# Performance work log

Hardware: AMD Instinct MI355X
Metric: run time of the kernel (lower is better)

The kernel has to match this reference:

```python
import jax, jax.numpy as jnp
import numpy as np

BETA = 0.05  # module hardcodes self.beta = 0.05 regardless of init arg
K = 4096
D = 512


def setup_inputs() -> dict:
    key = jax.random.key(0)
    k1, k2 = jax.random.split(key)
    latents = jax.random.normal(k1, (32, 1024, D), dtype=jnp.float32)
    # nn.Embedding weight init: normal_(mean=0.8, std=0.1)
    emb_weight = 0.8 + 0.1 * jax.random.normal(k2, (K, D), dtype=jnp.float32)
    return {"latents": latents, "emb_weight": emb_weight}


def reference(latents, emb_weight):
    B, S, Dm = latents.shape
    flat = latents.reshape(-1, Dm)  # [N, D]
    dist = (jnp.sum(flat * flat, axis=1, keepdims=True)
            + jnp.sum(emb_weight * emb_weight, axis=1)
            - 2.0 * jnp.matmul(flat, emb_weight.T))  # [N, K]
    inds = jnp.argmin(dist, axis=1)  # [N]
    quantized = emb_weight[inds].reshape(B, S, Dm)  # gather instead of one-hot matmul

    commitment_loss = jnp.mean((jax.lax.stop_gradient(quantized) - latents) ** 2)
    embedding_loss = jnp.mean((quantized - jax.lax.stop_gradient(latents)) ** 2)
    vq_loss = commitment_loss * BETA + embedding_loss

    # straight-through estimator
    quantized_st = latents + jax.lax.stop_gradient(quantized - latents)

    N = flat.shape[0]
    avg_probs = jnp.zeros((K,), dtype=latents.dtype).at[inds].add(1.0) / N
    perplexity = jnp.exp(-jnp.sum(avg_probs * jnp.log(avg_probs + 1e-10)))

    output_inds = inds.reshape(B, S)
    return (quantized_st, vq_loss, output_inds, emb_weight, perplexity)
```

## Files before the change

### kernel.cpp

```cpp
#include <hip/hip_runtime.h>
#include <cfloat>
#include <cmath>
#include <climits>
#include <cstdint>

#define N_ROWS   32768
#define D_DIM    512
#define K_CODES  4096

#define EPS_GAP  0.008f
#define CAND_WIN 0.02f
#define FLAG_CAP 12000

typedef short s16x8 __attribute__((ext_vector_type(8)));
typedef float f32x4 __attribute__((ext_vector_type(4)));


__device__ __forceinline__ short f2bf_rne(float x) {
    unsigned u = __float_as_uint(x);
    unsigned r = (u + 0x7fffu + ((u >> 16) & 1u)) >> 16;
    return (short)r;
}
__device__ __forceinline__ float bf2f(short b) {
    return __uint_as_float(((unsigned)(unsigned short)b) << 16);
}

__device__ __forceinline__ void gld16(const short* g, short* l) {
    __builtin_amdgcn_global_load_lds(
        reinterpret_cast<const __attribute__((address_space(1))) unsigned int*>(
            reinterpret_cast<uintptr_t>(g)),
        reinterpret_cast<__attribute__((address_space(3))) unsigned int*>(
            (unsigned int)(reinterpret_cast<uintptr_t>(l))),
        16, 0, 0);
}

__device__ __forceinline__ float np_block128_sq(const float* p) {
    float P[16];
    #pragma unroll
    for (int l = 0; l < 16; ++l) {
        float s0 = __fmul_rn(p[0 * 16 + l], p[0 * 16 + l]);
        float s1 = __fmul_rn(p[1 * 16 + l], p[1 * 16 + l]);
        float s2 = __fmul_rn(p[2 * 16 + l], p[2 * 16 + l]);
        float s3 = __fmul_rn(p[3 * 16 + l], p[3 * 16 + l]);
        float s4 = __fmul_rn(p[4 * 16 + l], p[4 * 16 + l]);
        float s5 = __fmul_rn(p[5 * 16 + l], p[5 * 16 + l]);
        float s6 = __fmul_rn(p[6 * 16 + l], p[6 * 16 + l]);
        float s7 = __fmul_rn(p[7 * 16 + l], p[7 * 16 + l]);
        float a01 = __fadd_rn(s0, s1);
        float a23 = __fadd_rn(s2, s3);
        float a45 = __fadd_rn(s4, s5);
        float a67 = __fadd_rn(s6, s7);
        P[l] = __fadd_rn(__fadd_rn(a01, a23), __fadd_rn(a45, a67));
    }
    float T3[8];
    #pragma unroll
    for (int k = 0; k < 8; ++k) T3[k] = __fadd_rn(P[k], P[k + 8]);
    float T6[4];
    #pragma unroll
    for (int k = 0; k < 4; ++k) T6[k] = __fadd_rn(T3[k], T3[k + 4]);
    return __fadd_rn(__fadd_rn(__fadd_rn(T6[0], T6[1]), T6[2]), T6[3]);
}
__device__ __forceinline__ float np_sum512_sq(const float* p) {
    float B0 = np_block128_sq(p);
    float B1 = np_block128_sq(p + 128);
    float B2 = np_block128_sq(p + 256);
    float B3 = np_block128_sq(p + 384);
    return __fadd_rn(__fadd_rn(B0, B1), __fadd_rn(B2, B3));
}

__global__ void vq_convert(const float* __restrict__ lat, const float* __restrict__ emb,
                           short* __restrict__ lat_hi, short* __restrict__ lat_lo,
                           short* __restrict__ emb_hi, short* __restrict__ emb_lo) {
    int i = blockIdx.x * 256 + threadIdx.x;
    const float* src; short *dh, *dl; size_t base;
    if (i < 2097152) { src = lat; dh = lat_hi; dl = lat_lo; base = (size_t)i * 8; }
    else             { src = emb; dh = emb_hi; dl = emb_lo; base = (size_t)(i - 2097152) * 8; }
    float4 a = *(const float4*)(src + base);
    float4 b = *(const float4*)(src + base + 4);
    float x[8] = {a.x, a.y, a.z, a.w, b.x, b.y, b.z, b.w};
    s16x8 hv, lv;
    #pragma unroll
    for (int j = 0; j < 8; ++j) {
        short h = f2bf_rne(x[j]);
        hv[j] = h;
        lv[j] = f2bf_rne(x[j] - bf2f(h));
    }
    *(s16x8*)(dh + base) = hv;
    *(s16x8*)(dl + base) = lv;
}

__global__ void vq_enorm(const float* __restrict__ emb, float* __restrict__ e_norm) {
    int item = blockIdx.x * 4 + (threadIdx.x >> 6);
    int lane = threadIdx.x & 63;
    const float4* s4 = (const float4*)(emb + (size_t)item * D_DIM);
    float4 a = s4[lane];
    float4 b = s4[64 + lane];
    float s = a.x * a.x + a.y * a.y + a.z * a.z + a.w * a.w
            + b.x * b.x + b.y * b.y + b.z * b.z + b.w * b.w;
    #pragma unroll
    for (int off = 32; off > 0; off >>= 1) s += __shfl_down(s, off);
    if (lane == 0) e_norm[item] = s;
}

__device__ __forceinline__ int kswz(int r) { return (r & 3) ^ ((r >> 2) & 3); }

#define BUFS 24576

__global__ __launch_bounds__(1024, 4)
void vq_argmin_mfma(const short* __restrict__ Ah_g, const short* __restrict__ Al_g,
                    const short* __restrict__ Bh_g, const short* __restrict__ Bl_g,
                    const float* __restrict__ e_norm,
                    unsigned short* __restrict__ fidx,
                    int* __restrict__ flagcnt, int* __restrict__ flaglist)
{
    __shared__ short smem[2 * BUFS];

    const int tid = threadIdx.x;
    const int l   = tid & 63;
    const int wid = tid >> 6;
    const int wr  = wid >> 2;
    const int wc  = wid & 3;
    const int l15 = l & 15;
    const int lhi = l >> 4;
    const int row0 = blockIdx.x * 128;

    float best[8], sec[8];
    int   bidx[8];
    #pragma unroll
    for (int s = 0; s < 8; ++s) { best[s] = FLT_MAX; sec[s] = FLT_MAX; bidx[s] = 0; }

    int offA[2], offB[4];
    #pragma unroll
    for (int m = 0; m < 2; ++m) {
        int r = wr * 32 + m * 16 + l15;
        offA[m] = r * 32 + (lhi ^ kswz(r)) * 8;
    }
    #pragma unroll
    for (int n = 0; n < 4; ++n) {
        int r = wc * 64 + n * 16 + l15;
        offB[n] = r * 32 + (lhi ^ kswz(r)) * 8;
    }

    const int  at   = tid & 511;
    const int  ar   = at >> 2, asl = at & 3;
    const bool aHi  = tid < 512;
    const short* Asrc = aHi ? Ah_g : Al_g;
    const int  adst = (aHi ? 0 : 4096) + at * 8;
    const size_t a_go0 = (size_t)(row0 + ar) * D_DIM + (asl ^ kswz(ar)) * 8;

    const int brr = tid >> 2, bsl = tid & 3;
    const int bko = (bsl ^ kswz(brr)) * 8;

    {
        gld16(Asrc + a_go0, smem + adst);
        size_t go = (size_t)brr * D_DIM + bko;
        gld16(Bh_g + go, smem + 8192 + tid * 8);
        gld16(Bl_g + go, smem + 16384 + tid * 8);
    }
    __syncthreads();

    f32x4 acc[2][4];
    #pragma unroll
    for (int m = 0; m < 2; ++m)
        #pragma unroll
        for (int n = 0; n < 4; ++n) acc[m][n] = (f32x4){0.f, 0.f, 0.f, 0.f};

    for (int s = 0; s < 256; ++s) {
        short* cur = smem + (s & 1) * BUFS;

        if (s < 255) {
            const int s1 = s + 1;
            const int k0 = (s1 & 15) * 32;
            const int cb0 = (s1 >> 4) * 256;
            short* nb = smem + (s1 & 1) * BUFS;
            gld16(Asrc + a_go0 + k0, nb + adst);
            size_t go = (size_t)(cb0 + brr) * D_DIM + k0 + bko;
            gld16(Bh_g + go, nb + 8192 + tid * 8);
            gld16(Bl_g + go, nb + 16384 + tid * 8);
        }

        s16x8 ah[2], al[2], bh[4], bl[4];
        #pragma unroll
        for (int m = 0; m < 2; ++m) {
            ah[m] = *(const s16x8*)(cur + offA[m]);
            al[m] = *(const s16x8*)(cur + 4096 + offA[m]);
        }
        #pragma unroll
        for (int n = 0; n < 4; ++n) {
            bh[n] = *(const s16x8*)(cur + 8192 + offB[n]);
            bl[n] = *(const s16x8*)(cur + 16384 + offB[n]);
        }

        #pragma unroll
        for (int m = 0; m < 2; ++m)
            #pragma unroll
            for (int n = 0; n < 4; ++n) {
                acc[m][n] = __builtin_amdgcn_mfma_f32_16x16x32_bf16(ah[m], bh[n], acc[m][n], 0, 0, 0);
                acc[m][n] = __builtin_amdgcn_mfma_f32_16x16x32_bf16(ah[m], bl[n], acc[m][n], 0, 0, 0);
                acc[m][n] = __builtin_amdgcn_mfma_f32_16x16x32_bf16(al[m], bh[n], acc[m][n], 0, 0, 0);
            }

        if ((s & 15) == 15) {
            const int cb0 = (s >> 4) * 256;
            #pragma unroll
            for (int n = 0; n < 4; ++n) {
                int c = cb0 + wc * 64 + n * 16 + l15;
                float en = e_norm[c];
                #pragma unroll
                for (int m = 0; m < 2; ++m)
                    #pragma unroll
                    for (int r = 0; r < 4; ++r) {
                        float dv = __fmaf_rn(-2.f, acc[m][n][r], en);
                        int si = m * 4 + r;
                        if (dv < best[si]) { sec[si] = best[si]; best[si] = dv; bidx[si] = c; }
                        else if (dv < sec[si]) sec[si] = dv;
                    }
            }
            #pragma unroll
            for (int m = 0; m < 2; ++m)
                #pragma unroll
                for (int n = 0; n < 4; ++n) acc[m][n] = (f32x4){0.f, 0.f, 0.f, 0.f};
        }

        __syncthreads();
    }

    #pragma unroll
    for (int s = 0; s < 8; ++s) {
        float v = best[s], sc = sec[s];
        int ix = bidx[s];
        #pragma unroll
        for (int off = 8; off > 0; off >>= 1) {
            float v2 = __shfl_xor(v, off);
            float s2 = __shfl_xor(sc, off);
            int   i2 = __shfl_xor(ix, off);
            float ns = fminf(fminf(sc, s2), fmaxf(v, v2));
            if (v2 < v || (v2 == v && i2 < ix)) { v = v2; ix = i2; }
            sc = ns;
        }
        best[s] = v; sec[s] = sc; bidx[s] = ix;
    }

    float* mb = (float*)smem;
    float* ms = mb + 512;
    int*   mi = (int*)(mb + 1024);
    if (l15 == 0) {
        #pragma unroll
        for (int m = 0; m < 2; ++m)
            #pragma unroll
            for (int r = 0; r < 4; ++r) {
                int s = m * 4 + r;
                int rowblk = wr * 32 + m * 16 + lhi * 4 + r;
                mb[wc * 128 + rowblk] = best[s];
                ms[wc * 128 + rowblk] = sec[s];
                mi[wc * 128 + rowblk] = bidx[s];
            }
    }
    __syncthreads();
    if (tid < 128) {
        float B = FLT_MAX, S = FLT_MAX;
        int I = 0;
        #pragma unroll
        for (int w = 0; w < 4; ++w) {
            float b = mb[w * 128 + tid], s = ms[w * 128 + tid];
            int i = mi[w * 128 + tid];
            if (b < B || (b == B && i < I)) { S = fminf(B, s); B = b; I = i; }
            else S = fminf(S, fminf(b, s));
        }
        int row = row0 + tid;
        fidx[row] = (unsigned short)I;
        if (S - B < EPS_GAP) {
            int p = atomicAdd(flagcnt, 1);
            if (p < FLAG_CAP) flaglist[p] = row;
        }
    }
}

#define FIXT 1024
#define NWAV 16
#define MAXC 128

__global__ __launch_bounds__(FIXT)
void vq_fixrow(const float* __restrict__ lat, const float* __restrict__ emb,
               const int* __restrict__ flagcnt, const int* __restrict__ flaglist,
               unsigned short* __restrict__ fidx)
{
    __shared__ float xs[D_DIM];
    __shared__ float dall[K_CODES];
    __shared__ float wmin_s[NWAV];
    __shared__ int   ccnt;
    __shared__ int   cands[MAXC];
    __shared__ float cd32[MAXC];

    const int t    = threadIdx.x;
    const int wave = t >> 6;
    const int lane = t & 63;
    int cnt = *flagcnt;
    if (cnt > FLAG_CAP) cnt = FLAG_CAP;

    for (int f = blockIdx.x; f < cnt; f += gridDim.x) {
        const int row = flaglist[f];
        __syncthreads();
        if (t < D_DIM) xs[t] = lat[(size_t)row * D_DIM + t];
        if (t == 0) ccnt = 0;
        __syncthreads();

        float x8[8];
        #pragma unroll
        for (int q = 0; q < 8; ++q) x8[q] = xs[lane * 8 + q];

        float lmin = FLT_MAX;
        for (int c = wave; c < K_CODES; c += 2 * NWAV) {
            const int c2 = c + NWAV;
            const float4* e4a = (const float4*)(emb + (size_t)c  * D_DIM);
            const float4* e4b = (const float4*)(emb + (size_t)c2 * D_DIM);
            float4 ea0 = e4a[lane * 2], ea1 = e4a[lane * 2 + 1];
            float4 eb0 = e4b[lane * 2], eb1 = e4b[lane * 2 + 1];

            float p0 = x8[0] - ea0.x, p1 = x8[1] - ea0.y;
            float p2 = x8[2] - ea0.z, p3 = x8[3] - ea0.w;
            float p4 = x8[4] - ea1.x, p5 = x8[5] - ea1.y;
            float p6 = x8[6] - ea1.z, p7 = x8[7] - ea1.w;
            float sA = __fmaf_rn(p0, p0, __fmaf_rn(p1, p1, __fmaf_rn(p2, p2, p3 * p3)));
            float sB = __fmaf_rn(p4, p4, __fmaf_rn(p5, p5, __fmaf_rn(p6, p6, p7 * p7)));
            float u = sA + sB;

            float q0 = x8[0] - eb0.x, q1 = x8[1] - eb0.y;
            float q2 = x8[2] - eb0.z, q3 = x8[3] - eb0.w;
            float q4 = x8[4] - eb1.x, q5 = x8[5] - eb1.y;
            float q6 = x8[6] - eb1.z, q7 = x8[7] - eb1.w;
            float tA = __fmaf_rn(q0, q0, __fmaf_rn(q1, q1, __fmaf_rn(q2, q2, q3 * q3)));
            float tB = __fmaf_rn(q4, q4, __fmaf_rn(q5, q5, __fmaf_rn(q6, q6, q7 * q7)));
            float v = tA + tB;

            #pragma unroll
            for (int off = 32; off > 0; off >>= 1) {
                u += __shfl_xor(u, off);
                v += __shfl_xor(v, off);
            }
            if (lane == 0) { dall[c] = u; dall[c2] = v; }
            lmin = fminf(lmin, fminf(u, v));
        }
        if (lane == 0) wmin_s[wave] = lmin;
        __syncthreads();

        float gmin = wmin_s[0];
        #pragma unroll
        for (int w = 1; w < NWAV; ++w) gmin = fminf(gmin, wmin_s[w]);
        const float thr = gmin + CAND_WIN;

        for (int c = t; c < K_CODES; c += FIXT) {
            if (dall[c] < thr) {
                int p = atomicAdd(&ccnt, 1);
                if (p < MAXC) cands[p] = c;
            }
        }
        __syncthreads();

        int nc = ccnt < MAXC ? ccnt : MAXC;
        if (t < nc) {
            int c = cands[t];
            const float* e = emb + (size_t)c * D_DIM;
            float t1 = np_sum512_sq(xs);
            float t2 = np_sum512_sq(e);
            float dot = 0.f;
            for (int k = 0; k < D_DIM; ++k)
                dot = __fmaf_rn(xs[k], e[k], dot);
            cd32[t] = __fsub_rn(__fadd_rn(t1, t2), __fmul_rn(2.f, dot));
        }
        __syncthreads();

        if (t == 0) {
            float bv = cd32[0]; int bx = cands[0];
            for (int w = 1; w < nc; ++w)
                if (cd32[w] < bv || (cd32[w] == bv && cands[w] < bx)) {
                    bv = cd32[w]; bx = cands[w];
                }
            fidx[row] = (unsigned short)bx;
        }
    }
}

__global__ void vq_gather(const float* __restrict__ lat, const float* __restrict__ emb,
                          const unsigned short* __restrict__ fidx,
                          float* __restrict__ out_q,
                          float* __restrict__ rowpart, int* __restrict__ hist) {
    int row  = blockIdx.x * 4 + (threadIdx.x >> 6);
    int lane = threadIdx.x & 63;
    int idx  = fidx[row];

    if (lane == 0) atomicAdd(&hist[idx], 1);

    const float4* e4 = (const float4*)(emb + (size_t)idx * D_DIM);
    const float4* x4 = (const float4*)(lat + (size_t)row * D_DIM);
    float4*       q4 = (float4*)(out_q + (size_t)row * D_DIM);

    float s = 0.f;
    #pragma unroll
    for (int i = 0; i < 2; ++i) {
        float4 e = e4[i * 64 + lane];
        float4 x = x4[i * 64 + lane];
        q4[i * 64 + lane] = e;
        float dx = e.x - x.x, dy = e.y - x.y, dz = e.z - x.z, dw = e.w - x.w;
        s += dx * dx + dy * dy + dz * dz + dw * dw;
    }
    #pragma unroll
    for (int off = 32; off > 0; off >>= 1) s += __shfl_down(s, off);
    if (lane == 0) rowpart[row] = s;
}

__global__ void vq_finalize(const float* __restrict__ rowpart, const int* __restrict__ hist,
                            float* __restrict__ out_loss, float* __restrict__ out_perp) {
    __shared__ float sdata[256];
    int t = threadIdx.x;

    float s = 0.f;
    for (int i = t; i < N_ROWS; i += 256) s += rowpart[i];
    sdata[t] = s;
    __syncthreads();
    for (int st = 128; st > 0; st >>= 1) {
        if (t < st) sdata[t] += sdata[t + st];
        __syncthreads();
    }
    if (t == 0) out_loss[0] = 1.05f * (sdata[0] / ((float)N_ROWS * (float)D_DIM));
    __syncthreads();

    float p = 0.f;
    for (int i = t; i < K_CODES; i += 256) {
        float pr = (float)hist[i] / (float)N_ROWS;
        p += pr * logf(pr + 1e-10f);
    }
    sdata[t] = p;
    __syncthreads();
    for (int st = 128; st > 0; st >>= 1) {
        if (t < st) sdata[t] += sdata[t + st];
        __syncthreads();
    }
    if (t == 0) out_perp[0] = expf(-sdata[0]);
}

__global__ void vq_inds(const unsigned short* __restrict__ fidx, float* __restrict__ out_inds) {
    int i = blockIdx.x * 1024 + threadIdx.x;
    out_inds[i] = (float)fidx[i];
}

extern "C" void kernel_launch(void* const* d_in, const int* in_sizes, int n_in,
                              void* d_out, int out_size, void* d_ws, size_t ws_size,
                              hipStream_t stream) {
    const float* lat = (const float*)d_in[0];
    const float* emb = (const float*)d_in[1];
    float* ob = (float*)d_out;

    short* emb_hi = (short*)(ob + 0);
    short* emb_lo = (short*)(ob + 1048576);
    short* lat_hi = (short*)(ob + 2097152);
    short* lat_lo = (short*)(ob + 10485760);
    float* e_norm = ob + 18874368;
    int*   flagcnt  = (int*)(ob + 18878464);
    int*   flaglist = (int*)(ob + 18878465);
    unsigned short* fidx = (unsigned short*)(ob + 18890496);
    int*   hist    = (int*)(ob + 16777220);
    float* rowpart = ob + 16781316;

    float* out_q    = ob;
    float* out_loss = ob + 16777216;
    float* out_inds = ob + 16777217;
    float* out_emb  = ob + 16809985;
    float* out_perp = ob + 18907137;

    hipMemsetAsync(flagcnt, 0, sizeof(int), stream);

    vq_convert<<<dim3(9216), dim3(256), 0, stream>>>(lat, emb, lat_hi, lat_lo, emb_hi, emb_lo);
    vq_enorm<<<dim3(1024), dim3(256), 0, stream>>>(emb, e_norm);

    vq_argmin_mfma<<<dim3(256), dim3(1024), 0, stream>>>(lat_hi, lat_lo, emb_hi, emb_lo,
                                                         e_norm, fidx, flagcnt, flaglist);

    hipMemsetAsync(hist, 0, K_CODES * sizeof(int), stream);

    vq_fixrow<<<dim3(512), dim3(FIXT), 0, stream>>>(lat, emb, flagcnt, flaglist, fidx);

    vq_gather<<<dim3(N_ROWS / 4), dim3(256), 0, stream>>>(lat, emb, fidx, out_q, rowpart, hist);

    vq_finalize<<<dim3(1), dim3(256), 0, stream>>>(rowpart, hist, out_loss, out_perp);

    vq_inds<<<dim3(32), dim3(1024), 0, stream>>>(fidx, out_inds);

    hipMemcpyAsync(out_emb, emb, (size_t)K_CODES * D_DIM * sizeof(float),
                   hipMemcpyDeviceToDevice, stream);
}
```

Baseline: 745.8 us.

## Triple-buffer LDS staging with partial vmcnt waits to prefetch two steps ahead

Expands the shared-memory staging area from two to three buffers and issues global-to-LDS loads two iterations ahead instead of one. The full __syncthreads at the end of each step becomes an explicit s_waitcnt vmcnt(3) plus s_barrier, so the next stage's loads can stay in flight across the barrier. The aim is to hide more global-memory latency behind the MFMA work. The cost is 144KB of LDS per block instead of 96KB, and correctness now depends on hand-counted vmcnt values matching the three loads each thread issues per stage.

```diff
diff --git a/kernel.cpp b/kernel.cpp
--- a/kernel.cpp
+++ b/kernel.cpp
@@ -113,7 +113,7 @@
                     unsigned short* __restrict__ fidx,
                     int* __restrict__ flagcnt, int* __restrict__ flaglist)
 {
-    __shared__ short smem[2 * BUFS];
+    __shared__ short smem[3 * BUFS];
 
     const int tid = threadIdx.x;
     const int l   = tid & 63;
@@ -151,13 +151,20 @@
     const int brr = tid >> 2, bsl = tid & 3;
     const int bko = (bsl ^ kswz(brr)) * 8;
 
-    {
-        gld16(Asrc + a_go0, smem + adst);
-        size_t go = (size_t)brr * D_DIM + bko;
-        gld16(Bh_g + go, smem + 8192 + tid * 8);
-        gld16(Bl_g + go, smem + 16384 + tid * 8);
-    }
-    __syncthreads();
+    auto STAGE = [&](int t, short* nb) {
+        const int k0  = (t & 15) * 32;
+        const int cb0 = (t >> 4) * 256;
+        gld16(Asrc + a_go0 + k0, nb + adst);
+        size_t go = (size_t)(cb0 + brr) * D_DIM + k0 + bko;
+        gld16(Bh_g + go, nb + 8192 + tid * 8);
+        gld16(Bl_g + go, nb + 16384 + tid * 8);
+    };
+
+    STAGE(0, smem);
+    STAGE(1, smem + BUFS);
+    asm volatile("s_waitcnt vmcnt(3)" ::: "memory");
+    __builtin_amdgcn_s_barrier();
+    __builtin_amdgcn_sched_barrier(0);
 
     f32x4 acc[2][4];
     #pragma unroll
@@ -165,18 +172,13 @@
         #pragma unroll
         for (int n = 0; n < 4; ++n) acc[m][n] = (f32x4){0.f, 0.f, 0.f, 0.f};
 
+    int cb = 0;
     for (int s = 0; s < 256; ++s) {
-        short* cur = smem + (s & 1) * BUFS;
-
-        if (s < 255) {
-            const int s1 = s + 1;
-            const int k0 = (s1 & 15) * 32;
-            const int cb0 = (s1 >> 4) * 256;
-            short* nb = smem + (s1 & 1) * BUFS;
-            gld16(Asrc + a_go0 + k0, nb + adst);
-            size_t go = (size_t)(cb0 + brr) * D_DIM + k0 + bko;
-            gld16(Bh_g + go, nb + 8192 + tid * 8);
-            gld16(Bl_g + go, nb + 16384 + tid * 8);
+        short* cur = smem + cb * BUFS;
+
+        if (s < 254) {
+            int nbi = cb + 2; if (nbi >= 3) nbi -= 3;
+            STAGE(s + 2, smem + nbi * BUFS);
         }
 
         s16x8 ah[2], al[2], bh[4], bl[4];
@@ -222,7 +224,15 @@
                 for (int n = 0; n < 4; ++n) acc[m][n] = (f32x4){0.f, 0.f, 0.f, 0.f};
         }
 
-        __syncthreads();
+        if (s >= 254) {
+            asm volatile("s_waitcnt vmcnt(0)" ::: "memory");
+        } else {
+            asm volatile("s_waitcnt vmcnt(3)" ::: "memory");
+        }
+        __builtin_amdgcn_s_barrier();
+        __builtin_amdgcn_sched_barrier(0);
+
+        cb = (cb + 1 == 3) ? 0 : cb + 1;
     }
 
     #pragma unroll
```

Result: no change. 754.3 us (+1.1%).
